# Performance work log

Measured on AMD Instinct MI355X. Metric: run time of the kernel, lower is better.

## Reference

```python
import jax, jax.numpy as jnp
import numpy as np

J = 25
C_IN, HID, LAT = 3, 64, 32


def _graph_conv(x, A, W, b):
    # x: [N,T,J,Cin]; A: [J,J]; W: [Cin,Cout]; b: [Cout]
    A = jax.nn.softmax(A, axis=-1)
    # fused adjacency mix + projection: (A @ x) @ W + b
    x = jnp.einsum('ij,ntjc->ntic', A, x)
    return jnp.einsum('ntjc,cd->ntjd', x, W) + b


def setup_inputs() -> dict:
    key = jax.random.key(0)
    ks = jax.random.split(key, 13)
    x = jax.random.normal(ks[0], (32, 2048, J, C_IN), dtype=jnp.float32)
    eye = jnp.eye(J, dtype=jnp.float32)
    def lin(kw, kb, cin, cout):
        W = jax.random.normal(kw, (cin, cout), dtype=jnp.float32) / np.sqrt(cin)
        b = jax.random.normal(kb, (cout,), dtype=jnp.float32) * 0.01
        return W, b
    W1, b1 = lin(ks[1], ks[2], C_IN, HID)
    W2, b2 = lin(ks[3], ks[4], HID, LAT)
    W3, b3 = lin(ks[5], ks[6], LAT, HID)
    W4, b4 = lin(ks[7], ks[8], HID, C_IN)
    return {
        'x': x,
        'A1': eye, 'W1': W1, 'b1': b1,
        'A2': eye, 'W2': W2, 'b2': b2,
        'A3': eye, 'W3': W3, 'b3': b3,
        'A4': eye, 'W4': W4, 'b4': b4,
    }


def reference(x, A1, W1, b1, A2, W2, b2, A3, W3, b3, A4, W4, b4):
    h = jax.nn.relu(_graph_conv(x, A1, W1, b1))     # encoder_g1 + relu
    z = _graph_conv(h, A2, W2, b2)                  # encoder_g2 (no relu)
    h_dec = jax.nn.relu(_graph_conv(z, A3, W3, b3)) # decoder_g1 + relu
    out = _graph_conv(h_dec, A4, W4, b4)            # decoder_g2
    return out
```

## Files before the change

### kernel.cpp

```cpp
#include <hip/hip_runtime.h>
#include <hip/hip_bf16.h>
#include <math.h>

#define J 25
#define NJC 75
#define NWAVE 4
#define NTHREADS 256
#define NFPW 4
#define SCRW 1056

#define O_A1T  0
#define O_APP  1024
#define O_A4B  2048
#define O_W2T  3072
#define O_W3T  5120
#define O_W1T  7168
#define O_W4C  8192
#define O_B4   8512
#define O_BPPF 8576

using bf16x8 = __attribute__((ext_vector_type(8))) __bf16;
using f32x4  = __attribute__((ext_vector_type(4))) float;
using f32x16 = __attribute__((ext_vector_type(16))) float;

__device__ inline bf16x8 zero8() {
    bf16x8 z;
    #pragma unroll
    for (int j = 0; j < 8; j++) z[j] = (__bf16)0.f;
    return z;
}

__device__ inline unsigned pk2(float a, float b) {
    float2 f2; f2.x = a; f2.y = b;
    __hip_bfloat162 h = __float22bfloat162_rn(f2);
    union { __hip_bfloat162 h2; unsigned u; } cv; cv.h2 = h;
    return cv.u;
}
__device__ inline bf16x8 mk8(unsigned a, unsigned b, unsigned c, unsigned d) {
    union { uint4 u4; bf16x8 v; } cv;
    cv.u4.x = a; cv.u4.y = b; cv.u4.z = c; cv.u4.w = d;
    return cv.v;
}
__device__ inline bf16x8 pk8(const f32x16& acc, int st) {
    const int b = 8 * st;
    return mk8(pk2(acc[b],     acc[b + 1]), pk2(acc[b + 2], acc[b + 3]),
               pk2(acc[b + 4], acc[b + 5]), pk2(acc[b + 6], acc[b + 7]));
}


__global__ void gcn_precompute(
    const float* __restrict__ A1, const float* __restrict__ W1, const float* __restrict__ b1,
    const float* __restrict__ A2, const float* __restrict__ W2, const float* __restrict__ b2,
    const float* __restrict__ A3, const float* __restrict__ W3, const float* __restrict__ b3,
    const float* __restrict__ A4, const float* __restrict__ W4, const float* __restrict__ b4,
    __bf16* __restrict__ cw)
{
    __shared__ float T[3125];
    __shared__ float bpp[64];
    float* T0 = T;        float* T1 = T + 625;  float* T2 = T + 1250;
    float* T3 = T + 1875; float* T4 = T + 2500;
    const int t = threadIdx.x;

    if (t < 100) {
        const int m = t / J, i = t % J;
        const float* Asrc = (m == 0) ? A1 : (m == 1) ? A2 : (m == 2) ? A3 : A4;
        float row[J];
        float mx = -1e30f;
        #pragma unroll
        for (int j = 0; j < J; j++) { row[j] = Asrc[i * J + j]; mx = fmaxf(mx, row[j]); }
        float s = 0.f;
        #pragma unroll
        for (int j = 0; j < J; j++) { row[j] = __expf(row[j] - mx); s += row[j]; }
        const float inv = 1.f / s;
        float* dst = T + m * 625 + i * J;
        #pragma unroll
        for (int j = 0; j < J; j++) dst[j] = row[j] * inv;
    }
    if (t < 64) {
        float s = b3[t];
        #pragma unroll
        for (int l = 0; l < 32; l++) s += W3[l * 64 + t] * b2[l];
        bpp[t] = s;
    }
    __syncthreads();

    for (int idx = t; idx < 625; idx += 256) {
        const int i = idx / J, jj = idx % J;
        float s = 0.f;
        #pragma unroll
        for (int k = 0; k < J; k++) s += T2[i * J + k] * T1[k * J + jj];
        T4[idx] = s;
    }
    __syncthreads();

    for (int i = t; i < 1024; i += 256) {
        const int b = i >> 8, n = (i >> 3) & 31, jj = i & 7;
        const int kn = 8 * b + jj;
        cw[O_A1T + i] = (__bf16)((kn < J && n < J) ? T0[n * J + kn] : 0.f);
        const int s = b >> 1, h = b & 1, r = 8 * s + jj;
        const int k32 = (r & 3) + 8 * (r >> 2) + 4 * h;
        cw[O_APP + i] = (__bf16)((k32 < J && n < J) ? T4[n * J + k32] : 0.f);
        cw[O_A4B + i] = (__bf16)((k32 < J && n < J) ? T3[n * J + k32] : 0.f);
    }
    for (int i = t; i < 2048; i += 256) {
        {
            const int b = i >> 8, n = (i >> 3) & 31, jj = i & 7;
            const int s = b >> 1, h = b & 1, r = 8 * (s & 1) + jj;
            const int d = 32 * (s >> 1) + (r & 3) + 8 * (r >> 2) + 4 * h;
            cw[O_W2T + i] = (__bf16)W2[d * 32 + n];
        }
        {
            const int tt = i >> 10, rr = i & 1023;
            const int b = rr >> 8, m = (rr >> 3) & 31, jj = rr & 7;
            const int s = b >> 1, h = b & 1, r = 8 * s + jj;
            const int l = (r & 3) + 8 * (r >> 2) + 4 * h;
            cw[O_W3T + i] = (__bf16)W3[l * 64 + tt * 32 + m];
        }
    }
    for (int i = t; i < 1024; i += 256) {
        const int tt = i >> 9, r = i & 511, hf = r >> 8, q = r & 255;
        const int m = q >> 3, c = q & 7, d = tt * 32 + m;
        float v = 0.f;
        if (hf == 0) {
            if (c < 3) v = W1[c * 64 + d];
            else if (c == 3) v = b1[d];
        }
        cw[O_W1T + i] = (__bf16)v;
    }
    if (t < 256) {
        const int c = t >> 6, b = (t >> 3) & 7, jj = t & 7;
        const int s = b >> 1, h = b & 1, r = 8 * (s & 1) + jj;
        const int d = 32 * (s >> 1) + (r & 3) + 8 * (r >> 2) + 4 * h;
        cw[O_W4C + t] = (c < 3) ? (__bf16)W4[d * 3 + c] : (__bf16)0.f;
    }
    {
        float* fwB = (float*)(cw + O_BPPF);
        if (t < 64) {
            const int q = t >> 4, h = (t >> 3) & 1, jj = t & 7;
            const int tt = q >> 1, st = q & 1;
            const int row32 = (jj & 3) + 16 * st + 8 * (jj >> 2) + 4 * h;
            fwB[t] = bpp[tt * 32 + row32];
        }
    }
    float* fb4 = (float*)(cw + O_B4);
    if (t >= 64 && t < 68) fb4[t - 64] = (t < 67) ? b4[t - 64] : 0.f;
}

__global__ __launch_bounds__(NTHREADS, 2) void gcn_fused(
    const float* __restrict__ x,
    const __bf16* __restrict__ cw,
    float* __restrict__ out)
{
    __shared__ __align__(16) __bf16 SCR[NWAVE * SCRW];

    const int t = threadIdx.x;
    const int w = t >> 6, lane = t & 63, ln = lane & 31, half = lane >> 5;
    const int fo = ln * 8;
    __bf16* sc = &SCR[w * SCRW];

    const long fbase = ((long)blockIdx.x * NWAVE + w) * NFPW;

    long xb = fbase * NJC;
    float xv0 = x[xb + lane];
    float xv1 = (lane < NJC - 64) ? x[xb + 64 + lane] : 0.f;

    if (half == 0) sc[(ln >> 3) * 264 + 24 + (ln & 7)] = (ln < J) ? (__bf16)1.f : (__bf16)0.f;
    if (lane < 21) sc[3 * 264 + (lane / 7) * 8 + 1 + (lane % 7)] = (__bf16)0.f;

    bf16x8 rA1T[2], rApp[2], rA4b[2], rW1[2], rW2[4], rW3[4], rW4[4];
    #pragma unroll
    for (int ks = 0; ks < 2; ks++) {
        rA1T[ks] = *(const bf16x8*)&cw[O_A1T + (2 * ks + half) * 256 + fo];
        rApp[ks] = *(const bf16x8*)&cw[O_APP + (2 * ks + half) * 256 + fo];
        rA4b[ks] = *(const bf16x8*)&cw[O_A4B + (2 * ks + half) * 256 + fo];
        rW1[ks]  = *(const bf16x8*)&cw[O_W1T + ks * 512 + half * 256 + fo];
    }
    #pragma unroll
    for (int ks = 0; ks < 4; ks++)
        rW2[ks] = *(const bf16x8*)&cw[O_W2T + (half + 2 * ks) * 256 + fo];
    #pragma unroll
    for (int tt = 0; tt < 2; tt++)
        #pragma unroll
        for (int ks = 0; ks < 2; ks++)
            rW3[tt * 2 + ks] = *(const bf16x8*)&cw[O_W3T + tt * 1024 + (half + 2 * ks) * 256 + fo];
    #pragma unroll
    for (int ks = 0; ks < 4; ks++) {
        rW4[ks] = zero8();
        if (ln < 3) rW4[ks] = *(const bf16x8*)&cw[O_W4C + ln * 64 + (half + 2 * ks) * 8];
    }
    f32x4 rBq[8];
    {
        const float* fwB = (const float*)(cw + O_BPPF);
        #pragma unroll
        for (int q = 0; q < 4; q++)
            #pragma unroll
            for (int p = 0; p < 2; p++)
                rBq[q * 2 + p] = *(const f32x4*)&fwB[(q * 2 + half) * 8 + 4 * p];
    }
    float b4v = 0.f;
    if (ln < 3) b4v = ((const float*)(cw + O_B4))[ln];

    f32x16 Z;
    #pragma unroll
    for (int z = 0; z < 16; z++) Z[z] = 0.f;

    const int c0 = lane % 3, j0 = lane / 3;
    const int sc0 = (j0 >> 3) * 264 + c0 * 8 + (j0 & 7);
    const int i1 = 64 + lane, c1 = i1 % 3, j1 = i1 / 3;
    const int sc1 = (j1 >> 3) * 264 + c1 * 8 + (j1 & 7);

    for (int fi = 0; fi < NFPW; fi++) {
        const long f = fbase + fi;

        sc[sc0] = (__bf16)xv0;
        if (lane < NJC - 64) sc[sc1] = (__bf16)xv1;

        float nxv0 = 0.f, nxv1 = 0.f;
        if (fi + 1 < NFPW) {
            const long nxb = (f + 1) * NJC;
            nxv0 = x[nxb + lane];
            if (lane < NJC - 64) nxv1 = x[nxb + 64 + lane];
        }

        bf16x8 a0 = *(const bf16x8*)&sc[half * 264 + fo];
        bf16x8 a1 = *(const bf16x8*)&sc[(2 + half) * 264 + fo];
        f32x16 accY = __builtin_amdgcn_mfma_f32_32x32x16_bf16(a0, rA1T[0], Z, 0, 0, 0);
        accY = __builtin_amdgcn_mfma_f32_32x32x16_bf16(a1, rA1T[1], accY, 0, 0, 0);

        bf16x8 yb;
        #pragma unroll
        for (int jj = 0; jj < 8; jj++)
            yb[jj] = (half == 0 && jj < 4) ? (__bf16)accY[jj] : (__bf16)0.f;
        bf16x8 hf[4];
        #pragma unroll
        for (int tt = 0; tt < 2; tt++) {
            f32x16 acc = __builtin_amdgcn_mfma_f32_32x32x16_bf16(rW1[tt], yb, Z, 0, 0, 0);
            #pragma unroll
            for (int z = 0; z < 16; z++) acc[z] = fmaxf(acc[z], 0.f);
            hf[2 * tt]     = pk8(acc, 0);
            hf[2 * tt + 1] = pk8(acc, 1);
        }

        f32x16 accU = __builtin_amdgcn_mfma_f32_32x32x16_bf16(hf[0], rW2[0], Z, 0, 0, 0);
        #pragma unroll
        for (int s = 1; s < 4; s++)
            accU = __builtin_amdgcn_mfma_f32_32x32x16_bf16(hf[s], rW2[s], accU, 0, 0, 0);
        bf16x8 uf[2] = { pk8(accU, 0), pk8(accU, 1) };

        f32x16 accV = __builtin_amdgcn_mfma_f32_32x32x16_bf16(uf[0], rApp[0], Z, 0, 0, 0);
        accV = __builtin_amdgcn_mfma_f32_32x32x16_bf16(uf[1], rApp[1], accV, 0, 0, 0);
        bf16x8 vf[2] = { pk8(accV, 0), pk8(accV, 1) };

        bf16x8 hd[4];
        #pragma unroll
        for (int tt = 0; tt < 2; tt++) {
            f32x16 acc = __builtin_amdgcn_mfma_f32_32x32x16_bf16(rW3[tt * 2 + 0], vf[0], Z, 0, 0, 0);
            acc = __builtin_amdgcn_mfma_f32_32x32x16_bf16(rW3[tt * 2 + 1], vf[1], acc, 0, 0, 0);
            #pragma unroll
            for (int st = 0; st < 2; st++) {
                const int q = 2 * tt + st;
                #pragma unroll
                for (int jj = 0; jj < 8; jj++)
                    acc[8 * st + jj] = fmaxf(acc[8 * st + jj] + rBq[q * 2 + (jj >> 2)][jj & 3], 0.f);
                hd[q] = pk8(acc, st);
            }
        }

        f32x16 accP = __builtin_amdgcn_mfma_f32_32x32x16_bf16(hd[0], rW4[0], Z, 0, 0, 0);
        #pragma unroll
        for (int s = 1; s < 4; s++)
            accP = __builtin_amdgcn_mfma_f32_32x32x16_bf16(hd[s], rW4[s], accP, 0, 0, 0);
        bf16x8 pf[2] = { pk8(accP, 0), pk8(accP, 1) };

        f32x16 accO = __builtin_amdgcn_mfma_f32_32x32x16_bf16(rA4b[0], pf[0], Z, 0, 0, 0);
        accO = __builtin_amdgcn_mfma_f32_32x32x16_bf16(rA4b[1], pf[1], accO, 0, 0, 0);
        if (ln < 3) {
            const long ob = f * NJC;
            #pragma unroll
            for (int r = 0; r < 16; r++) {
                const int row = (r & 3) + 8 * (r >> 2) + 4 * half;
                if (row < J) out[ob + row * 3 + ln] = accO[r] + b4v;
            }
        }

        xv0 = nxv0; xv1 = nxv1;
    }
}

extern "C" void kernel_launch(void* const* d_in, const int* in_sizes, int n_in,
                              void* d_out, int out_size, void* d_ws, size_t ws_size,
                              hipStream_t stream)
{
    const float* x  = (const float*)d_in[0];
    const float* A1 = (const float*)d_in[1];
    const float* W1 = (const float*)d_in[2];
    const float* b1 = (const float*)d_in[3];
    const float* A2 = (const float*)d_in[4];
    const float* W2 = (const float*)d_in[5];
    const float* b2 = (const float*)d_in[6];
    const float* A3 = (const float*)d_in[7];
    const float* W3 = (const float*)d_in[8];
    const float* b3 = (const float*)d_in[9];
    const float* A4 = (const float*)d_in[10];
    const float* W4 = (const float*)d_in[11];
    const float* b4 = (const float*)d_in[12];
    float* out = (float*)d_out;
    __bf16* cw = (__bf16*)d_ws;

    const int NT = in_sizes[0] / NJC;
    const int nblocks = NT / (NWAVE * NFPW);

    gcn_precompute<<<1, 256, 0, stream>>>(
        A1, W1, b1, A2, W2, b2, A3, W3, b3, A4, W4, b4, cw);
    gcn_fused<<<nblocks, NTHREADS, 0, stream>>>(x, cw, out);
}
```

Measured before the change: 154.1 us.

## Double-buffer per-wave LDS input tile and use packed bf16 conversion builtin

Doubles the per-wave LDS scratch into two buffers, so the next frame's input is written into the alternate buffer while the current one is read. The global prefetch now runs two frames ahead, which is meant to hide the LDS write-to-read dependency and the global load latency. It also replaces the HIP bf16x2 conversion helper with the packed cvt_pk_bf16_f32 builtin when the compiler provides it, cutting instruction count in the pack steps. LDS use per block doubles, which could lower occupancy.

```diff
diff --git a/kernel.cpp b/kernel.cpp
--- a/kernel.cpp
+++ b/kernel.cpp
@@ -1,5 +1,4 @@
 #include <hip/hip_runtime.h>
-#include <hip/hip_bf16.h>
 #include <math.h>
 
 #define J 25
@@ -7,7 +6,7 @@
 #define NWAVE 4
 #define NTHREADS 256
 #define NFPW 4
-#define SCRW 1056
+#define SCRW 2112
 
 #define O_A1T  0
 #define O_APP  1024
@@ -19,6 +18,7 @@
 #define O_B4   8512
 #define O_BPPF 8576
 
+using bf16x2 = __attribute__((ext_vector_type(2))) __bf16;
 using bf16x8 = __attribute__((ext_vector_type(8))) __bf16;
 using f32x4  = __attribute__((ext_vector_type(4))) float;
 using f32x16 = __attribute__((ext_vector_type(16))) float;
@@ -30,21 +30,28 @@
     return z;
 }
 
-__device__ inline unsigned pk2(float a, float b) {
-    float2 f2; f2.x = a; f2.y = b;
-    __hip_bfloat162 h = __float22bfloat162_rn(f2);
-    union { __hip_bfloat162 h2; unsigned u; } cv; cv.h2 = h;
-    return cv.u;
-}
-__device__ inline bf16x8 mk8(unsigned a, unsigned b, unsigned c, unsigned d) {
-    union { uint4 u4; bf16x8 v; } cv;
-    cv.u4.x = a; cv.u4.y = b; cv.u4.z = c; cv.u4.w = d;
-    return cv.v;
+#if defined(__has_builtin)
+#if __has_builtin(__builtin_amdgcn_cvt_pk_bf16_f32)
+#define HAVE_PK_BF16 1
+#endif
+#endif
+
+__device__ inline bf16x2 cvt2(float a, float b) {
+#ifdef HAVE_PK_BF16
+    return __builtin_amdgcn_cvt_pk_bf16_f32(a, b);
+#else
+    bf16x2 r; r[0] = (__bf16)a; r[1] = (__bf16)b; return r;
+#endif
 }
 __device__ inline bf16x8 pk8(const f32x16& acc, int st) {
     const int b = 8 * st;
-    return mk8(pk2(acc[b],     acc[b + 1]), pk2(acc[b + 2], acc[b + 3]),
-               pk2(acc[b + 4], acc[b + 5]), pk2(acc[b + 6], acc[b + 7]));
+    bf16x8 r;
+    #pragma unroll
+    for (int p = 0; p < 4; p++) {
+        bf16x2 v = cvt2(acc[b + 2 * p], acc[b + 2 * p + 1]);
+        r[2 * p] = v[0]; r[2 * p + 1] = v[1];
+    }
+    return r;
 }
 
 
@@ -136,8 +143,8 @@
     {
         float* fwB = (float*)(cw + O_BPPF);
         if (t < 64) {
-            const int q = t >> 4, h = (t >> 3) & 1, jj = t & 7;
-            const int tt = q >> 1, st = q & 1;
+            const int g = t >> 4, h = (t >> 3) & 1, jj = t & 7;
+            const int tt = g >> 1, st = g & 1;
             const int row32 = (jj & 3) + 16 * st + 8 * (jj >> 2) + 4 * h;
             fwB[t] = bpp[tt * 32 + row32];
         }
@@ -156,16 +163,35 @@
     const int t = threadIdx.x;
     const int w = t >> 6, lane = t & 63, ln = lane & 31, half = lane >> 5;
     const int fo = ln * 8;
-    __bf16* sc = &SCR[w * SCRW];
+    __bf16* scr = &SCR[w * SCRW];
 
     const long fbase = ((long)blockIdx.x * NWAVE + w) * NFPW;
 
-    long xb = fbase * NJC;
-    float xv0 = x[xb + lane];
-    float xv1 = (lane < NJC - 64) ? x[xb + 64 + lane] : 0.f;
-
-    if (half == 0) sc[(ln >> 3) * 264 + 24 + (ln & 7)] = (ln < J) ? (__bf16)1.f : (__bf16)0.f;
-    if (lane < 21) sc[3 * 264 + (lane / 7) * 8 + 1 + (lane % 7)] = (__bf16)0.f;
+    #pragma unroll
+    for (int r = 0; r < 2; r++) {
+        __bf16* s = scr + r * 1056;
+        if (half == 0) s[(ln >> 3) * 264 + 24 + (ln & 7)] = (ln < J) ? (__bf16)1.f : (__bf16)0.f;
+        if (lane < 21) s[3 * 264 + (lane / 7) * 8 + 1 + (lane % 7)] = (__bf16)0.f;
+    }
+
+    const int c0 = lane % 3, j0 = lane / 3;
+    const int sx0 = (j0 >> 3) * 264 + c0 * 8 + (j0 & 7);
+    const int i1 = 64 + lane, c1 = i1 % 3, j1 = i1 / 3;
+    const int sx1 = (j1 >> 3) * 264 + c1 * 8 + (j1 & 7);
+
+    {
+        const long xb = fbase * NJC;
+        float v0 = x[xb + lane];
+        float v1 = (lane < NJC - 64) ? x[xb + 64 + lane] : 0.f;
+        scr[sx0] = (__bf16)v0;
+        if (lane < NJC - 64) scr[sx1] = (__bf16)v1;
+    }
+    float xv0 = 0.f, xv1 = 0.f;
+    if (NFPW > 1) {
+        const long xb = (fbase + 1) * NJC;
+        xv0 = x[xb + lane];
+        if (lane < NJC - 64) xv1 = x[xb + 64 + lane];
+    }
 
     bf16x8 rA1T[2], rApp[2], rA4b[2], rW1[2], rW2[4], rW3[4], rW4[4];
     #pragma unroll
@@ -192,10 +218,10 @@
     {
         const float* fwB = (const float*)(cw + O_BPPF);
         #pragma unroll
-        for (int q = 0; q < 4; q++)
+        for (int g = 0; g < 4; g++)
             #pragma unroll
             for (int p = 0; p < 2; p++)
-                rBq[q * 2 + p] = *(const f32x4*)&fwB[(q * 2 + half) * 8 + 4 * p];
+                rBq[g * 2 + p] = *(const f32x4*)&fwB[(g * 2 + half) * 8 + 4 * p];
     }
     float b4v = 0.f;
     if (ln < 3) b4v = ((const float*)(cw + O_B4))[ln];
@@ -204,22 +230,19 @@
     #pragma unroll
     for (int z = 0; z < 16; z++) Z[z] = 0.f;
 
-    const int c0 = lane % 3, j0 = lane / 3;
-    const int sc0 = (j0 >> 3) * 264 + c0 * 8 + (j0 & 7);
-    const int i1 = 64 + lane, c1 = i1 % 3, j1 = i1 / 3;
-    const int sc1 = (j1 >> 3) * 264 + c1 * 8 + (j1 & 7);
-
     for (int fi = 0; fi < NFPW; fi++) {
         const long f = fbase + fi;
-
-        sc[sc0] = (__bf16)xv0;
-        if (lane < NJC - 64) sc[sc1] = (__bf16)xv1;
-
-        float nxv0 = 0.f, nxv1 = 0.f;
+        __bf16* sc = scr + (fi & 1) * 1056;
+
         if (fi + 1 < NFPW) {
-            const long nxb = (f + 1) * NJC;
-            nxv0 = x[nxb + lane];
-            if (lane < NJC - 64) nxv1 = x[nxb + 64 + lane];
+            __bf16* sn = scr + ((fi + 1) & 1) * 1056;
+            sn[sx0] = (__bf16)xv0;
+            if (lane < NJC - 64) sn[sx1] = (__bf16)xv1;
+        }
+        if (fi + 2 < NFPW) {
+            const long nxb = (f + 2) * NJC;
+            xv0 = x[nxb + lane];
+            if (lane < NJC - 64) xv1 = x[nxb + 64 + lane];
         }
 
         bf16x8 a0 = *(const bf16x8*)&sc[half * 264 + fo];
@@ -227,10 +250,12 @@
         f32x16 accY = __builtin_amdgcn_mfma_f32_32x32x16_bf16(a0, rA1T[0], Z, 0, 0, 0);
         accY = __builtin_amdgcn_mfma_f32_32x32x16_bf16(a1, rA1T[1], accY, 0, 0, 0);
 
-        bf16x8 yb;
-        #pragma unroll
-        for (int jj = 0; jj < 8; jj++)
-            yb[jj] = (half == 0 && jj < 4) ? (__bf16)accY[jj] : (__bf16)0.f;
+        bf16x8 yb = zero8();
+        if (half == 0) {
+            bf16x2 q0 = cvt2(accY[0], accY[1]);
+            bf16x2 q1 = cvt2(accY[2], accY[3]);
+            yb[0] = q0[0]; yb[1] = q0[1]; yb[2] = q1[0]; yb[3] = q1[1];
+        }
         bf16x8 hf[4];
         #pragma unroll
         for (int tt = 0; tt < 2; tt++) {
@@ -258,11 +283,11 @@
             acc = __builtin_amdgcn_mfma_f32_32x32x16_bf16(rW3[tt * 2 + 1], vf[1], acc, 0, 0, 0);
             #pragma unroll
             for (int st = 0; st < 2; st++) {
-                const int q = 2 * tt + st;
+                const int g = 2 * tt + st;
                 #pragma unroll
                 for (int jj = 0; jj < 8; jj++)
-                    acc[8 * st + jj] = fmaxf(acc[8 * st + jj] + rBq[q * 2 + (jj >> 2)][jj & 3], 0.f);
-                hd[q] = pk8(acc, st);
+                    acc[8 * st + jj] = fmaxf(acc[8 * st + jj] + rBq[g * 2 + (jj >> 2)][jj & 3], 0.f);
+                hd[g] = pk8(acc, st);
             }
         }
 
@@ -282,8 +307,6 @@
                 if (row < J) out[ob + row * 3 + ln] = accO[r] + b4v;
             }
         }
-
-        xv0 = nxv0; xv1 = nxv1;
     }
 }
 
```

Result: faster. 145.3 us (-5.7%).
